# Kernel tuning notes

Measured on AMD Instinct MI355X. Metric: run time of the kernel, lower is better.

The kernel has to match this reference:

```python
import jax, jax.numpy as jnp
import numpy as np

ENC = 768
DEC = 768
B, T, S = 16, 1024, 1024


def setup_inputs() -> dict:
    key = jax.random.key(0)
    k1, k2, k3 = jax.random.split(key, 3)
    inputs = jax.random.normal(k1, (B, T, DEC), dtype=jnp.float32)
    context = jax.random.normal(k2, (B, S, ENC), dtype=jnp.float32)
    # linear_out: Linear(dec+enc -> dec) with bias; torch weight layout [out, in]
    W_out = jax.random.normal(k3, (DEC, DEC + ENC), dtype=jnp.float32) * 0.02
    b_out = jnp.zeros((DEC,), dtype=jnp.float32)
    w_scale = jnp.ones((1, 1, 1), dtype=jnp.float32)   # self.weight
    b_scale = jnp.ones((1, 1, 1), dtype=jnp.float32)   # self.bias
    prelu_a = jnp.full((1,), 0.25, dtype=jnp.float32)  # PReLU single param
    return {"inputs": inputs, "context": context, "W_out": W_out,
            "b_out": b_out, "w_scale": w_scale, "b_scale": b_scale,
            "prelu_a": prelu_a}


def reference(inputs, context, W_out, b_out, w_scale, b_scale, prelu_a):
    # score: bmm(h_t, h_s^T). NOTE: linear_in output is discarded in the
    # original (h_t reassigned), so the raw inputs are used — faithful here.
    align = jnp.einsum('btd,bsd->bts', inputs, context)        # [B,T,S]
    av = jax.nn.softmax(align, axis=-1)                        # softmax over src
    # gate: sigmoid of per-source column-sum over target positions
    gate = jax.nn.sigmoid(jnp.sum(av, axis=1, keepdims=True))  # [B,1,S]
    # AdaptiveAvgPool1d(1): mean over last (src) dim -> [B,T,1]
    pooled = jnp.mean(av, axis=-1, keepdims=True)
    av_g = av * gate * pooled                                  # fused elementwise
    c = jnp.einsum('bts,bsd->btd', av_g, context)              # [B,T,ENC]
    c = c * w_scale + b_scale                                  # scalar affine
    concat_c = jnp.concatenate([c, inputs], axis=-1)           # [B,T,ENC+DEC]
    h = jnp.einsum('btk,dk->btd', concat_c, W_out) + b_out     # linear_out
    attn_h = jnp.where(h >= 0, h, prelu_a * h)                 # PReLU
    return attn_h.transpose(1, 0, 2), av_g.transpose(1, 0, 2)
```

## Files before the change

kernel.cpp:

```cpp
#include <hip/hip_runtime.h>

#define B_ 16
#define T_ 1024
#define S_ 1024
#define D_ 768
#define K3_ 1536
#define BS_ (B_ * S_)
#define BD_ (B_ * D_)
#define BPAD_ 40
#define NI_ (B_ * T_ * D_)
#define NW_ (D_ * K3_)

typedef __attribute__((ext_vector_type(8))) _Float16 half8;
typedef __attribute__((ext_vector_type(4))) float float4v;

__device__ __forceinline__ unsigned short f2h(float x) {
    return __builtin_bit_cast(unsigned short, (_Float16)x);
}
__device__ __forceinline__ float h2f(unsigned short u) {
    return (float)__builtin_bit_cast(_Float16, u);
}
__device__ __forceinline__ unsigned pkh2(float a, float b) {
    return (unsigned)f2h(a) | ((unsigned)f2h(b) << 16);
}
__device__ __forceinline__ uint2 pkh4(const float4 v) {
    return make_uint2(pkh2(v.x, v.y), pkh2(v.z, v.w));
}

#define MFMA_PROLOG() \
    const int tid  = threadIdx.x; \
    const int w    = tid >> 6; \
    const int wm   = (w >> 1) * 64; \
    const int wn   = (w & 1) * 64; \
    const int lane = tid & 63; \
    const int q    = lane >> 4; \
    const int lr   = lane & 15; \
    const int arow = tid >> 1; \
    const int acg  = (tid & 1) * 16; \
    float4v acc[4][4] = {};

#define MFMA_COMPUTE_F16() \
    { \
        half8 afr[4], bfr[4]; \
        _Pragma("unroll") \
        for (int i = 0; i < 4; i++) \
            afr[i] = *(const half8*)&As[(wm + i * 16 + lr) * BPAD_ + q * 8]; \
        _Pragma("unroll") \
        for (int j = 0; j < 4; j++) \
            bfr[j] = *(const half8*)&Bs[(wn + j * 16 + lr) * BPAD_ + q * 8]; \
        _Pragma("unroll") \
        for (int i = 0; i < 4; i++) \
            _Pragma("unroll") \
            for (int j = 0; j < 4; j++) \
                acc[i][j] = __builtin_amdgcn_mfma_f32_16x16x32_f16( \
                    afr[i], bfr[j], acc[i][j], 0, 0, 0); \
    }

__global__ __launch_bounds__(256) void prep_h(
    const float* __restrict__ inp, const float* __restrict__ W,
    unsigned short* __restrict__ inp_h, unsigned short* __restrict__ W_h)
{
    const size_t i4 = (size_t)blockIdx.x * 256 + threadIdx.x;
    const size_t flat = i4 * 4;
    float4 v;
    unsigned short* dst;
    if (flat < NI_) {
        v = ((const float4*)inp)[i4];
        dst = inp_h + flat;
    } else {
        v = *(const float4*)(W + (flat - NI_));
        dst = W_h + (flat - NI_);
    }
    *(uint2*)dst = pkh4(v);
}

__global__ __launch_bounds__(256) void transpose_ctx(
    const float* __restrict__ ctx, unsigned short* __restrict__ ctxT,
    unsigned short* __restrict__ ctx_h)
{
    const int b  = blockIdx.z;
    const int d0 = blockIdx.y * 64;
    const int s0 = blockIdx.x * 64;
    __shared__ unsigned short Ts[64 * 68];

    const int tid = threadIdx.x;
    const int srel = tid >> 4;
    const int dcol = (tid & 15) * 4;
#pragma unroll
    for (int r = 0; r < 4; r++) {
        const int s = srel + r * 16;
        float4 v = *(const float4*)(ctx + ((size_t)b * S_ + s0 + s) * D_ + d0 + dcol);
        Ts[(dcol + 0) * 68 + s] = f2h(v.x);
        Ts[(dcol + 1) * 68 + s] = f2h(v.y);
        Ts[(dcol + 2) * 68 + s] = f2h(v.z);
        Ts[(dcol + 3) * 68 + s] = f2h(v.w);
        *(uint2*)(ctx_h + ((size_t)b * S_ + s0 + s) * D_ + d0 + dcol) = pkh4(v);
    }
    __syncthreads();
    const int drow = tid >> 2;
    const int scg  = (tid & 3) * 16;
    unsigned short* dst = ctxT + ((size_t)b * D_ + d0 + drow) * S_ + s0 + scg;
#pragma unroll
    for (int p = 0; p < 4; p++) {
        uint2 u = *(const uint2*)&Ts[drow * 68 + scg + p * 4];
        *(uint2*)(dst + p * 4) = u;
    }
}

__global__ __launch_bounds__(256) void gemm_scores_f16(
    const unsigned short* __restrict__ ctx_h,
    const unsigned short* __restrict__ inp_h,
    float* __restrict__ out2)
{
    const int b  = blockIdx.z;
    const int t0 = blockIdx.y * 128;
    const int s0 = blockIdx.x * 128;

    __shared__ __align__(16) unsigned short As[128 * BPAD_];
    __shared__ __align__(16) unsigned short Bs[128 * BPAD_];

    MFMA_PROLOG();

    const unsigned short* asrc = ctx_h + ((size_t)b * S_ + s0 + arow) * D_;
    const unsigned short* bsrc = inp_h + ((size_t)b * T_ + t0 + arow) * D_;

    for (int kb = 0; kb < D_; kb += 32) {
        const uint4 a0 = ((const uint4*)(asrc + kb + acg))[0];
        const uint4 a1 = ((const uint4*)(asrc + kb + acg))[1];
        const uint4 b0 = ((const uint4*)(bsrc + kb + acg))[0];
        const uint4 b1 = ((const uint4*)(bsrc + kb + acg))[1];
        __syncthreads();
        *(uint4*)&As[arow * BPAD_ + acg]     = a0;
        *(uint4*)&As[arow * BPAD_ + acg + 8] = a1;
        *(uint4*)&Bs[arow * BPAD_ + acg]     = b0;
        *(uint4*)&Bs[arow * BPAD_ + acg + 8] = b1;
        __syncthreads();
        MFMA_COMPUTE_F16();
    }

#pragma unroll
    for (int i = 0; i < 4; i++)
#pragma unroll
        for (int j = 0; j < 4; j++) {
            const int t = t0 + wn + j * 16 + lr;
            const int s = s0 + wm + i * 16 + q * 4;
            *(float4v*)(out2 + (size_t)t * BS_ + (size_t)b * S_ + s) = acc[i][j];
        }
}

__global__ __launch_bounds__(256) void softmax_rows(
    const float* __restrict__ scores, unsigned short* __restrict__ av_h)
{
    const int bid = blockIdx.x;
    const int b = bid & (B_ - 1);
    const int t = bid / B_;
    const float* row = scores + (size_t)t * BS_ + (size_t)b * S_;
    const int tid = threadIdx.x;

    float4 v = ((const float4*)row)[tid];
    float m = fmaxf(fmaxf(v.x, v.y), fmaxf(v.z, v.w));
#pragma unroll
    for (int off = 32; off > 0; off >>= 1) m = fmaxf(m, __shfl_xor(m, off));

    __shared__ float red[8];
    if ((tid & 63) == 0) red[tid >> 6] = m;
    __syncthreads();
    m = fmaxf(fmaxf(red[0], red[1]), fmaxf(red[2], red[3]));

    float4 e;
    e.x = __expf(v.x - m); e.y = __expf(v.y - m);
    e.z = __expf(v.z - m); e.w = __expf(v.w - m);
    float s = e.x + e.y + e.z + e.w;
#pragma unroll
    for (int off = 32; off > 0; off >>= 1) s += __shfl_xor(s, off);
    if ((tid & 63) == 0) red[4 + (tid >> 6)] = s;
    __syncthreads();
    s = (red[4] + red[5]) + (red[6] + red[7]);

    const float inv = 1.0f / s;
    e.x *= inv; e.y *= inv; e.z *= inv; e.w *= inv;
    unsigned short* orow = av_h + (size_t)t * BS_ + (size_t)b * S_;
    *(uint2*)(orow + tid * 4) = pkh4(e);
}

__global__ __launch_bounds__(256) void colsum_part(
    const unsigned short* __restrict__ av_h, float* __restrict__ partial)
{
    const int b = blockIdx.y;
    const int c = blockIdx.z;
    const int s2 = blockIdx.x * 512 + threadIdx.x * 2;
    const unsigned short* p = av_h + (size_t)(c * 128) * BS_ + (size_t)b * S_ + s2;
    float s0 = 0.0f, s1 = 0.0f;
#pragma unroll 8
    for (int t = 0; t < 128; t++) {
        const unsigned u = *(const unsigned*)(p + (size_t)t * BS_);
        s0 += h2f((unsigned short)(u & 0xffff));
        s1 += h2f((unsigned short)(u >> 16));
    }
    *(float2*)(partial + ((size_t)c * B_ + b) * S_ + s2) = make_float2(s0, s1);
}

__global__ __launch_bounds__(256) void gate_final(
    const float* __restrict__ partial, float* __restrict__ gate)
{
    const int idx = blockIdx.x * 256 + threadIdx.x;
    const int b = idx >> 10, s = idx & (S_ - 1);
    float sum = 0.0f;
#pragma unroll
    for (int c = 0; c < T_ / 128; c++) sum += partial[((size_t)c * B_ + b) * S_ + s];
    gate[idx] = (1.0f / (1.0f + __expf(-sum))) * (1.0f / (float)S_);
}

__global__ __launch_bounds__(256) void av_out(
    const unsigned short* __restrict__ av_h, const float* __restrict__ gate,
    float* __restrict__ out2)
{
    const size_t i8 = ((size_t)blockIdx.x * 256 + threadIdx.x) * 8;
    const int s = (int)(i8 & (S_ - 1));
    const int b = (int)((i8 >> 10) & (B_ - 1));
    const uint4 u = *(const uint4*)(av_h + i8);
    const float4 g0 = *(const float4*)(gate + b * S_ + s);
    const float4 g1 = *(const float4*)(gate + b * S_ + s + 4);
    float4 o0 = make_float4(h2f(u.x & 0xffff) * g0.x, h2f(u.x >> 16) * g0.y,
                            h2f(u.y & 0xffff) * g0.z, h2f(u.y >> 16) * g0.w);
    float4 o1 = make_float4(h2f(u.z & 0xffff) * g1.x, h2f(u.z >> 16) * g1.y,
                            h2f(u.w & 0xffff) * g1.z, h2f(u.w >> 16) * g1.w);
    *(float4*)(out2 + i8) = o0;
    *(float4*)(out2 + i8 + 4) = o1;
}

__global__ __launch_bounds__(256) void scale_ctxT(
    unsigned short* __restrict__ ctxT, const float* __restrict__ gate)
{
    const int b = blockIdx.y;
    const int d = blockIdx.x * 2 + (threadIdx.x >> 7);
    const int s = (threadIdx.x & 127) * 8;
    unsigned short* p = ctxT + ((size_t)b * D_ + d) * S_ + s;
    const uint4 u = *(const uint4*)p;
    const float4 g0 = *(const float4*)(gate + b * S_ + s);
    const float4 g1 = *(const float4*)(gate + b * S_ + s + 4);
    uint4 o;
    o.x = pkh2(h2f(u.x & 0xffff) * g0.x, h2f(u.x >> 16) * g0.y);
    o.y = pkh2(h2f(u.y & 0xffff) * g0.z, h2f(u.y >> 16) * g0.w);
    o.z = pkh2(h2f(u.z & 0xffff) * g1.x, h2f(u.z >> 16) * g1.y);
    o.w = pkh2(h2f(u.w & 0xffff) * g1.z, h2f(u.w >> 16) * g1.w);
    *(uint4*)p = o;
}

__global__ __launch_bounds__(256) void gemm_ctx_f16(
    const unsigned short* __restrict__ ctxT, const unsigned short* __restrict__ av_h,
    const float* __restrict__ w_scale, const float* __restrict__ b_scale,
    unsigned short* __restrict__ c_h)
{
    const int b  = blockIdx.z;
    const int d0 = blockIdx.y * 128;
    const int t0 = blockIdx.x * 128;

    __shared__ __align__(16) unsigned short As[128 * BPAD_];
    __shared__ __align__(16) unsigned short Bs[128 * BPAD_];

    MFMA_PROLOG();

    const unsigned short* asrc = ctxT + ((size_t)b * D_ + d0 + arow) * S_;
    const unsigned short* bsrc = av_h + (size_t)(t0 + arow) * BS_ + (size_t)b * S_;

    for (int sb = 0; sb < S_; sb += 32) {
        const uint4 a0 = ((const uint4*)(asrc + sb + acg))[0];
        const uint4 a1 = ((const uint4*)(asrc + sb + acg))[1];
        const uint4 b0 = ((const uint4*)(bsrc + sb + acg))[0];
        const uint4 b1 = ((const uint4*)(bsrc + sb + acg))[1];
        __syncthreads();
        *(uint4*)&As[arow * BPAD_ + acg]     = a0;
        *(uint4*)&As[arow * BPAD_ + acg + 8] = a1;
        *(uint4*)&Bs[arow * BPAD_ + acg]     = b0;
        *(uint4*)&Bs[arow * BPAD_ + acg + 8] = b1;
        __syncthreads();
        MFMA_COMPUTE_F16();
    }

    const float wsc = w_scale[0], bsc = b_scale[0];
#pragma unroll
    for (int i = 0; i < 4; i++)
#pragma unroll
        for (int j = 0; j < 4; j++) {
            const int d = d0 + wm + i * 16 + q * 4;
            const int t = t0 + wn + j * 16 + lr;
            uint2 o;
            o.x = pkh2(acc[i][j][0] * wsc + bsc, acc[i][j][1] * wsc + bsc);
            o.y = pkh2(acc[i][j][2] * wsc + bsc, acc[i][j][3] * wsc + bsc);
            *(uint2*)(c_h + ((size_t)b * T_ + t) * D_ + d) = o;
        }
}

__global__ __launch_bounds__(256) void gemm_out_f16(
    const unsigned short* __restrict__ c_h, const unsigned short* __restrict__ inp_h,
    const unsigned short* __restrict__ W_h, const float* __restrict__ bias,
    const float* __restrict__ prelu_a, float* __restrict__ out0)
{
    const int n0 = blockIdx.x * 128;
    const int d0 = blockIdx.y * 128;

    __shared__ __align__(16) unsigned short As[128 * BPAD_];
    __shared__ __align__(16) unsigned short Bs[128 * BPAD_];

    MFMA_PROLOG();

    const unsigned short* asrc = W_h + (size_t)(d0 + arow) * K3_;

    for (int kb = 0; kb < K3_; kb += 32) {
        const uint4 a0 = ((const uint4*)(asrc + kb + acg))[0];
        const uint4 a1 = ((const uint4*)(asrc + kb + acg))[1];
        const unsigned short* bp = (kb < D_)
            ? c_h   + (size_t)(n0 + arow) * D_ + kb + acg
            : inp_h + (size_t)(n0 + arow) * D_ + (kb - D_) + acg;
        const uint4 b0 = ((const uint4*)bp)[0];
        const uint4 b1 = ((const uint4*)bp)[1];
        __syncthreads();
        *(uint4*)&As[arow * BPAD_ + acg]     = a0;
        *(uint4*)&As[arow * BPAD_ + acg + 8] = a1;
        *(uint4*)&Bs[arow * BPAD_ + acg]     = b0;
        *(uint4*)&Bs[arow * BPAD_ + acg + 8] = b1;
        __syncthreads();
        MFMA_COMPUTE_F16();
    }

    const float pa = prelu_a[0];
#pragma unroll
    for (int i = 0; i < 4; i++) {
        const int d = d0 + wm + i * 16 + q * 4;
        const float4 bz = *(const float4*)(bias + d);
#pragma unroll
        for (int j = 0; j < 4; j++) {
            const int n = n0 + wn + j * 16 + lr;
            const int bb = n >> 10;
            const int t = n & (T_ - 1);
            float4 h;
            h.x = acc[i][j][0] + bz.x;
            h.y = acc[i][j][1] + bz.y;
            h.z = acc[i][j][2] + bz.z;
            h.w = acc[i][j][3] + bz.w;
            h.x = h.x >= 0.0f ? h.x : pa * h.x;
            h.y = h.y >= 0.0f ? h.y : pa * h.y;
            h.z = h.z >= 0.0f ? h.z : pa * h.z;
            h.w = h.w >= 0.0f ? h.w : pa * h.w;
            *(float4*)(out0 + (size_t)t * BD_ + (size_t)bb * D_ + d) = h;
        }
    }
}

extern "C" void kernel_launch(void* const* d_in, const int* in_sizes, int n_in,
                              void* d_out, int out_size, void* d_ws, size_t ws_size,
                              hipStream_t stream)
{
    const float* inputs  = (const float*)d_in[0];
    const float* context = (const float*)d_in[1];
    const float* W_out   = (const float*)d_in[2];
    const float* b_out   = (const float*)d_in[3];
    const float* w_scale = (const float*)d_in[4];
    const float* b_scale = (const float*)d_in[5];
    const float* prelu_a = (const float*)d_in[6];

    float* out0 = (float*)d_out;
    float* out2 = out0 + (size_t)T_ * B_ * D_;

    unsigned short* c_h   = (unsigned short*)d_ws;
    unsigned short* ctxT  = c_h   + (size_t)B_ * T_ * D_;
    unsigned short* av_h  = ctxT  + (size_t)B_ * D_ * S_;
    unsigned short* inp_h = av_h  + (size_t)T_ * B_ * S_;
    unsigned short* W_h   = inp_h + (size_t)B_ * T_ * D_;
    float* gate    = (float*)(W_h + (size_t)NW_);
    float* partial = gate + (size_t)B_ * S_;

    prep_h<<<(NI_ + NW_) / 4 / 256, 256, 0, stream>>>(inputs, W_out, inp_h, W_h);
    transpose_ctx<<<dim3(S_ / 64, D_ / 64, B_), 256, 0, stream>>>(context, ctxT, c_h);
    gemm_scores_f16<<<dim3(S_ / 128, T_ / 128, B_), 256, 0, stream>>>(
        c_h , inp_h, out2);
    softmax_rows<<<B_ * T_, 256, 0, stream>>>(out2, av_h);
    colsum_part<<<dim3(S_ / 512, B_, T_ / 128), 256, 0, stream>>>(av_h, partial);
    gate_final<<<(B_ * S_) / 256, 256, 0, stream>>>(partial, gate);
    av_out<<<(int)(((size_t)T_ * B_ * S_ / 8) / 256), 256, 0, stream>>>(av_h, gate, out2);
    scale_ctxT<<<dim3(D_ / 2, B_), 256, 0, stream>>>(ctxT, gate);
    gemm_ctx_f16<<<dim3(T_ / 128, D_ / 128, B_), 256, 0, stream>>>(
        ctxT, av_h, w_scale, b_scale, c_h);
    gemm_out_f16<<<dim3((B_ * T_) / 128, D_ / 128), 256, 0, stream>>>(
        c_h, inp_h, W_h, b_out, prelu_a, out0);
}
```

Before: 439.1 us.

## Stage GEMM tiles via direct global-to-LDS loads and merge prep kernels

The three f16 MFMA GEMMs now move their A/B tiles straight from global memory into LDS with global_load_lds (16-byte per lane), instead of loading into registers and then writing to padded shared memory. The LDS tiles become unpadded with a 32-element row stride, which may add bank conflicts on the fragment reads. Separately, the context transpose and the input/weight f16 conversion kernels are merged into a single launch to save one kernel launch. There is still no double buffering, so load latency remains exposed between barriers.

```diff
diff --git a/kernel.cpp b/kernel.cpp
--- a/kernel.cpp
+++ b/kernel.cpp
@@ -7,7 +7,6 @@
 #define K3_ 1536
 #define BS_ (B_ * S_)
 #define BD_ (B_ * D_)
-#define BPAD_ 40
 #define NI_ (B_ * T_ * D_)
 #define NW_ (D_ * K3_)
 
@@ -25,6 +24,13 @@
 }
 __device__ __forceinline__ uint2 pkh4(const float4 v) {
     return make_uint2(pkh2(v.x, v.y), pkh2(v.z, v.w));
+}
+
+__device__ __forceinline__ void gl_lds16(const void* g, void* l) {
+    __builtin_amdgcn_global_load_lds(
+        (const __attribute__((address_space(1))) unsigned int*)g,
+        (__attribute__((address_space(3))) unsigned int*)l,
+        16, 0, 0);
 }
 
 #define MFMA_PROLOG() \
@@ -35,19 +41,25 @@
     const int lane = tid & 63; \
     const int q    = lane >> 4; \
     const int lr   = lane & 15; \
-    const int arow = tid >> 1; \
-    const int acg  = (tid & 1) * 16; \
     float4v acc[4][4] = {};
+
+#define STAGE_PROLOG() \
+    const int rl0 = (w << 5) + (lane >> 2); \
+    const int cc  = (lane & 3) * 8; \
+    unsigned short* const Aw0 = &As[w * 1024]; \
+    unsigned short* const Aw1 = &As[w * 1024 + 512]; \
+    unsigned short* const Bw0 = &Bs[w * 1024]; \
+    unsigned short* const Bw1 = &Bs[w * 1024 + 512];
 
 #define MFMA_COMPUTE_F16() \
     { \
         half8 afr[4], bfr[4]; \
         _Pragma("unroll") \
         for (int i = 0; i < 4; i++) \
-            afr[i] = *(const half8*)&As[(wm + i * 16 + lr) * BPAD_ + q * 8]; \
+            afr[i] = *(const half8*)&As[(wm + i * 16 + lr) * 32 + q * 8]; \
         _Pragma("unroll") \
         for (int j = 0; j < 4; j++) \
-            bfr[j] = *(const half8*)&Bs[(wn + j * 16 + lr) * BPAD_ + q * 8]; \
+            bfr[j] = *(const half8*)&Bs[(wn + j * 16 + lr) * 32 + q * 8]; \
         _Pragma("unroll") \
         for (int i = 0; i < 4; i++) \
             _Pragma("unroll") \
@@ -56,54 +68,54 @@
                     afr[i], bfr[j], acc[i][j], 0, 0, 0); \
     }
 
-__global__ __launch_bounds__(256) void prep_h(
-    const float* __restrict__ inp, const float* __restrict__ W,
+__global__ __launch_bounds__(256) void prep_all(
+    const float* __restrict__ ctx, const float* __restrict__ inp,
+    const float* __restrict__ W,
+    unsigned short* __restrict__ ctxT, unsigned short* __restrict__ ctx_h,
     unsigned short* __restrict__ inp_h, unsigned short* __restrict__ W_h)
 {
-    const size_t i4 = (size_t)blockIdx.x * 256 + threadIdx.x;
-    const size_t flat = i4 * 4;
-    float4 v;
-    unsigned short* dst;
-    if (flat < NI_) {
-        v = ((const float4*)inp)[i4];
-        dst = inp_h + flat;
+    __shared__ unsigned short Ts[64 * 68];
+    const int bid = blockIdx.x;
+    const int tid = threadIdx.x;
+    if (bid < 3072) {
+        const int b   = bid / 192;
+        const int rem = bid - b * 192;
+        const int d0  = (rem >> 4) * 64;
+        const int s0  = (rem & 15) * 64;
+        const int srel = tid >> 4;
+        const int dcol = (tid & 15) * 4;
+#pragma unroll
+        for (int r = 0; r < 4; r++) {
+            const int s = srel + r * 16;
+            float4 v = *(const float4*)(ctx + ((size_t)b * S_ + s0 + s) * D_ + d0 + dcol);
+            Ts[(dcol + 0) * 68 + s] = f2h(v.x);
+            Ts[(dcol + 1) * 68 + s] = f2h(v.y);
+            Ts[(dcol + 2) * 68 + s] = f2h(v.z);
+            Ts[(dcol + 3) * 68 + s] = f2h(v.w);
+            *(uint2*)(ctx_h + ((size_t)b * S_ + s0 + s) * D_ + d0 + dcol) = pkh4(v);
+        }
+        __syncthreads();
+        const int drow = tid >> 2;
+        const int scg  = (tid & 3) * 16;
+        unsigned short* dst = ctxT + ((size_t)b * D_ + d0 + drow) * S_ + s0 + scg;
+#pragma unroll
+        for (int p = 0; p < 4; p++) {
+            uint2 u = *(const uint2*)&Ts[drow * 68 + scg + p * 4];
+            *(uint2*)(dst + p * 4) = u;
+        }
     } else {
-        v = *(const float4*)(W + (flat - NI_));
-        dst = W_h + (flat - NI_);
-    }
-    *(uint2*)dst = pkh4(v);
-}
-
-__global__ __launch_bounds__(256) void transpose_ctx(
-    const float* __restrict__ ctx, unsigned short* __restrict__ ctxT,
-    unsigned short* __restrict__ ctx_h)
-{
-    const int b  = blockIdx.z;
-    const int d0 = blockIdx.y * 64;
-    const int s0 = blockIdx.x * 64;
-    __shared__ unsigned short Ts[64 * 68];
-
-    const int tid = threadIdx.x;
-    const int srel = tid >> 4;
-    const int dcol = (tid & 15) * 4;
-#pragma unroll
-    for (int r = 0; r < 4; r++) {
-        const int s = srel + r * 16;
-        float4 v = *(const float4*)(ctx + ((size_t)b * S_ + s0 + s) * D_ + d0 + dcol);
-        Ts[(dcol + 0) * 68 + s] = f2h(v.x);
-        Ts[(dcol + 1) * 68 + s] = f2h(v.y);
-        Ts[(dcol + 2) * 68 + s] = f2h(v.z);
-        Ts[(dcol + 3) * 68 + s] = f2h(v.w);
-        *(uint2*)(ctx_h + ((size_t)b * S_ + s0 + s) * D_ + d0 + dcol) = pkh4(v);
-    }
-    __syncthreads();
-    const int drow = tid >> 2;
-    const int scg  = (tid & 3) * 16;
-    unsigned short* dst = ctxT + ((size_t)b * D_ + d0 + drow) * S_ + s0 + scg;
-#pragma unroll
-    for (int p = 0; p < 4; p++) {
-        uint2 u = *(const uint2*)&Ts[drow * 68 + scg + p * 4];
-        *(uint2*)(dst + p * 4) = u;
+        const size_t i4 = (size_t)(bid - 3072) * 256 + tid;
+        const size_t flat = i4 * 4;
+        float4 v;
+        unsigned short* dst;
+        if (flat < NI_) {
+            v = ((const float4*)inp)[i4];
+            dst = inp_h + flat;
+        } else {
+            v = *(const float4*)(W + (flat - NI_));
+            dst = W_h + (flat - NI_);
+        }
+        *(uint2*)dst = pkh4(v);
     }
 }
 
@@ -116,24 +128,23 @@
     const int t0 = blockIdx.y * 128;
     const int s0 = blockIdx.x * 128;
 
-    __shared__ __align__(16) unsigned short As[128 * BPAD_];
-    __shared__ __align__(16) unsigned short Bs[128 * BPAD_];
+    __shared__ __align__(16) unsigned short As[128 * 32];
+    __shared__ __align__(16) unsigned short Bs[128 * 32];
 
     MFMA_PROLOG();
-
-    const unsigned short* asrc = ctx_h + ((size_t)b * S_ + s0 + arow) * D_;
-    const unsigned short* bsrc = inp_h + ((size_t)b * T_ + t0 + arow) * D_;
+    STAGE_PROLOG();
+
+    const unsigned short* ga0 = ctx_h + ((size_t)b * S_ + s0 + rl0) * D_ + cc;
+    const unsigned short* ga1 = ga0 + (size_t)16 * D_;
+    const unsigned short* gb0 = inp_h + ((size_t)b * T_ + t0 + rl0) * D_ + cc;
+    const unsigned short* gb1 = gb0 + (size_t)16 * D_;
 
     for (int kb = 0; kb < D_; kb += 32) {
-        const uint4 a0 = ((const uint4*)(asrc + kb + acg))[0];
-        const uint4 a1 = ((const uint4*)(asrc + kb + acg))[1];
-        const uint4 b0 = ((const uint4*)(bsrc + kb + acg))[0];
-        const uint4 b1 = ((const uint4*)(bsrc + kb + acg))[1];
-        __syncthreads();
-        *(uint4*)&As[arow * BPAD_ + acg]     = a0;
-        *(uint4*)&As[arow * BPAD_ + acg + 8] = a1;
-        *(uint4*)&Bs[arow * BPAD_ + acg]     = b0;
-        *(uint4*)&Bs[arow * BPAD_ + acg + 8] = b1;
+        __syncthreads();
+        gl_lds16(ga0 + kb, Aw0);
+        gl_lds16(ga1 + kb, Aw1);
+        gl_lds16(gb0 + kb, Bw0);
+        gl_lds16(gb1 + kb, Bw1);
         __syncthreads();
         MFMA_COMPUTE_F16();
     }
@@ -256,24 +267,23 @@
     const int d0 = blockIdx.y * 128;
     const int t0 = blockIdx.x * 128;
 
-    __shared__ __align__(16) unsigned short As[128 * BPAD_];
-    __shared__ __align__(16) unsigned short Bs[128 * BPAD_];
+    __shared__ __align__(16) unsigned short As[128 * 32];
+    __shared__ __align__(16) unsigned short Bs[128 * 32];
 
     MFMA_PROLOG();
-
-    const unsigned short* asrc = ctxT + ((size_t)b * D_ + d0 + arow) * S_;
-    const unsigned short* bsrc = av_h + (size_t)(t0 + arow) * BS_ + (size_t)b * S_;
+    STAGE_PROLOG();
+
+    const unsigned short* ga0 = ctxT + ((size_t)b * D_ + d0 + rl0) * S_ + cc;
+    const unsigned short* ga1 = ga0 + (size_t)16 * S_;
+    const unsigned short* gb0 = av_h + (size_t)(t0 + rl0) * BS_ + (size_t)b * S_ + cc;
+    const unsigned short* gb1 = gb0 + (size_t)16 * BS_;
 
     for (int sb = 0; sb < S_; sb += 32) {
-        const uint4 a0 = ((const uint4*)(asrc + sb + acg))[0];
-        const uint4 a1 = ((const uint4*)(asrc + sb + acg))[1];
-        const uint4 b0 = ((const uint4*)(bsrc + sb + acg))[0];
-        const uint4 b1 = ((const uint4*)(bsrc + sb + acg))[1];
-        __syncthreads();
-        *(uint4*)&As[arow * BPAD_ + acg]     = a0;
-        *(uint4*)&As[arow * BPAD_ + acg + 8] = a1;
-        *(uint4*)&Bs[arow * BPAD_ + acg]     = b0;
-        *(uint4*)&Bs[arow * BPAD_ + acg + 8] = b1;
+        __syncthreads();
+        gl_lds16(ga0 + sb, Aw0);
+        gl_lds16(ga1 + sb, Aw1);
+        gl_lds16(gb0 + sb, Bw0);
+        gl_lds16(gb1 + sb, Bw1);
         __syncthreads();
         MFMA_COMPUTE_F16();
     }
@@ -300,26 +310,25 @@
     const int n0 = blockIdx.x * 128;
     const int d0 = blockIdx.y * 128;
 
-    __shared__ __align__(16) unsigned short As[128 * BPAD_];
-    __shared__ __align__(16) unsigned short Bs[128 * BPAD_];
+    __shared__ __align__(16) unsigned short As[128 * 32];
+    __shared__ __align__(16) unsigned short Bs[128 * 32];
 
     MFMA_PROLOG();
-
-    const unsigned short* asrc = W_h + (size_t)(d0 + arow) * K3_;
+    STAGE_PROLOG();
+
+    const unsigned short* ga0  = W_h + (size_t)(d0 + rl0) * K3_ + cc;
+    const unsigned short* ga1  = ga0 + (size_t)16 * K3_;
+    const unsigned short* gbc0 = c_h + (size_t)(n0 + rl0) * D_ + cc;
+    const unsigned short* gbi0 = inp_h + (size_t)(n0 + rl0) * D_ + cc;
 
     for (int kb = 0; kb < K3_; kb += 32) {
-        const uint4 a0 = ((const uint4*)(asrc + kb + acg))[0];
-        const uint4 a1 = ((const uint4*)(asrc + kb + acg))[1];
-        const unsigned short* bp = (kb < D_)
-            ? c_h   + (size_t)(n0 + arow) * D_ + kb + acg
-            : inp_h + (size_t)(n0 + arow) * D_ + (kb - D_) + acg;
-        const uint4 b0 = ((const uint4*)bp)[0];
-        const uint4 b1 = ((const uint4*)bp)[1];
-        __syncthreads();
-        *(uint4*)&As[arow * BPAD_ + acg]     = a0;
-        *(uint4*)&As[arow * BPAD_ + acg + 8] = a1;
-        *(uint4*)&Bs[arow * BPAD_ + acg]     = b0;
-        *(uint4*)&Bs[arow * BPAD_ + acg + 8] = b1;
+        const unsigned short* gb0 = (kb < D_) ? gbc0 + kb : gbi0 + (kb - D_);
+        const unsigned short* gb1 = gb0 + (size_t)16 * D_;
+        __syncthreads();
+        gl_lds16(ga0 + kb, Aw0);
+        gl_lds16(ga1 + kb, Aw1);
+        gl_lds16(gb0, Bw0);
+        gl_lds16(gb1, Bw1);
         __syncthreads();
         MFMA_COMPUTE_F16();
     }
@@ -371,8 +380,8 @@
     float* gate    = (float*)(W_h + (size_t)NW_);
     float* partial = gate + (size_t)B_ * S_;
 
-    prep_h<<<(NI_ + NW_) / 4 / 256, 256, 0, stream>>>(inputs, W_out, inp_h, W_h);
-    transpose_ctx<<<dim3(S_ / 64, D_ / 64, B_), 256, 0, stream>>>(context, ctxT, c_h);
+    prep_all<<<3072 + (NI_ + NW_) / 4 / 256, 256, 0, stream>>>(
+        context, inputs, W_out, ctxT, c_h, inp_h, W_h);
     gemm_scores_f16<<<dim3(S_ / 128, T_ / 128, B_), 256, 0, stream>>>(
         c_h , inp_h, out2);
     softmax_rows<<<B_ * T_, 256, 0, stream>>>(out2, av_h);
```

New measurement: 391.3 us. 10.9% less time.
